# Performance work log

Measured on AMD Instinct MI355X. Metric: run time of the kernel, lower is better.

The kernel has to match this reference:

```python
import jax, jax.numpy as jnp
import numpy as np

HIDDEN = 384
HEADS = 8
DIM_HEAD = HIDDEN // HEADS  # 48
INNER = DIM_HEAD * HEADS
SCALE = DIM_HEAD ** -0.5


def setup_inputs() -> dict:
    key = jax.random.key(0)
    k1, k2, k3, k4 = jax.random.split(key, 4)
    B, C, D, H, W = 2, HIDDEN, 16, 16, 8
    x = jax.random.normal(k1, (B, C, D, H, W), dtype=jnp.float32)
    # nn.Linear weights (stored as [out, in] in torch; use [in, out] here)
    w_qkv = jax.random.normal(k2, (C, 3 * INNER), dtype=jnp.float32) * (C ** -0.5)
    w_out = jax.random.normal(k3, (INNER, C), dtype=jnp.float32) * (INNER ** -0.5)
    b_out = jax.random.normal(k4, (C,), dtype=jnp.float32) * 0.02
    return {"x": x, "w_qkv": w_qkv, "w_out": w_out, "b_out": b_out}


def reference(x, w_qkv, w_out, b_out):
    B, C, D, H, W = x.shape
    N = D * H * W
    tokens = x.reshape(B, C, N).transpose(0, 2, 1)          # [B, N, C]
    qkv = tokens @ w_qkv                                     # [B, N, 3*inner]
    qkv = qkv.reshape(B, N, 3, HEADS, DIM_HEAD).transpose(2, 0, 3, 1, 4)
    q, k, v = qkv[0], qkv[1], qkv[2]                         # [B, h, N, dh]
    q = jnp.clip(q, -5.0, 5.0)
    k = jnp.clip(k, -5.0, 5.0)
    logits = jnp.einsum('bhnd,bhmd->bhnm', q, k) * SCALE     # [B, h, N, N]
    logits = logits - jnp.max(logits, axis=-1, keepdims=True)
    attn = jax.nn.softmax(logits, axis=-1)
    out = jnp.einsum('bhnm,bhmd->bhnd', attn, v)             # [B, h, N, dh]
    out = out.transpose(0, 2, 1, 3).reshape(B, N, INNER)     # [B, N, inner]
    out = out @ w_out + b_out                                # [B, N, C]
    out = out.transpose(0, 2, 1).reshape(B, C, D, H, W)
    return x + out
```

## Files before the change

kernel.cpp:

```cpp
#include <hip/hip_runtime.h>

#define B_SZ 2
#define C_IN 384
#define N_TOK 2048
#define HEADS 8
#define DH 48
#define J3 1152
#define QSCALE_LOG2 0.20823509110768f
#define KSPLIT 4
#define KEYS_PER_SPLIT 512
#define DEFER_THR 11.0f

typedef __attribute__((ext_vector_type(8))) _Float16 f16x8;
typedef __attribute__((ext_vector_type(4))) _Float16 f16x4;
typedef __attribute__((ext_vector_type(4))) float f32x4;

__device__ __forceinline__ unsigned short f2h(float f) {
  _Float16 h = (_Float16)f;
  return __builtin_bit_cast(unsigned short, h);
}
__device__ __forceinline__ uint pk2(float a, float b) {
  return __builtin_bit_cast(uint, __builtin_amdgcn_cvt_pkrtz(a, b));
}
__device__ __forceinline__ float exp2g(float x) {
  return __builtin_amdgcn_exp2f(x);
}

__global__ __launch_bounds__(256) void tr_kernel(
    const float* __restrict__ x, const float* __restrict__ wq,
    const float* __restrict__ wo, unsigned short* __restrict__ xh,
    unsigned short* __restrict__ wqh, unsigned short* __restrict__ woh) {
  const int z = blockIdx.z;
  const float* src;
  unsigned short* dst;
  int C;
  if (z < 2) {
    src = x + (size_t)z * C_IN * N_TOK;
    dst = xh + (size_t)z * N_TOK * C_IN;
    C = N_TOK;
  } else if (z == 2) {
    src = wq; dst = wqh; C = J3;
  } else {
    src = wo; dst = woh; C = C_IN;
  }
  const int c0 = blockIdx.x * 64;
  const int r0 = blockIdx.y * 64;
  if (c0 >= C) return;
  __shared__ unsigned short T[64][74];
  const int tid = threadIdx.x;
  const int cc = tid & 63;
#pragma unroll
  for (int i = 0; i < 16; ++i) {
    const int rr = 4 * i + (tid >> 6);
    T[cc][rr] = f2h(src[(size_t)(r0 + rr) * C + c0 + cc]);
  }
  __syncthreads();
  const int cc2 = tid >> 2;
  const int seg = (tid & 3) * 16;
  uint v[8];
#pragma unroll
  for (int k = 0; k < 8; ++k)
    v[k] = (uint)T[cc2][seg + 2 * k] | ((uint)T[cc2][seg + 2 * k + 1] << 16);
  unsigned short* dp = dst + (size_t)(c0 + cc2) * C_IN + r0 + seg;
  *(uint4*)dp = make_uint4(v[0], v[1], v[2], v[3]);
  *(uint4*)(dp + 8) = make_uint4(v[4], v[5], v[6], v[7]);
}

__global__ __launch_bounds__(256) void qkv_mfma(
    const unsigned short* __restrict__ xh, const unsigned short* __restrict__ wqh,
    unsigned short* __restrict__ Qo, unsigned short* __restrict__ Ko,
    unsigned short* __restrict__ Vo) {
  __shared__ __align__(16) unsigned short Ts[128][72];
  __shared__ __align__(16) unsigned short Ws[64][72];
  const int tid = threadIdx.x;
  const int w = tid >> 6, lane = tid & 63;
  const int lc = lane & 15, lg = lane >> 4;
  const int m0 = blockIdx.x * 128;
  const int j0 = blockIdx.y * 64;
  const int b = m0 >> 11;

  f32x4 acc[2][4];
#pragma unroll
  for (int i = 0; i < 2; ++i)
#pragma unroll
    for (int j = 0; j < 4; ++j) acc[i][j] = (f32x4){0.f, 0.f, 0.f, 0.f};

  const int trow = tid & 127, tseg = tid >> 7;
  const int wrow = tid & 63,  wseg = tid >> 6;

  for (int kk = 0; kk < C_IN; kk += 64) {
    {
      const uint4* s = (const uint4*)(xh + (size_t)(m0 + trow) * C_IN + kk + tseg * 32);
      uint4* d = (uint4*)&Ts[trow][tseg * 32];
      d[0] = s[0]; d[1] = s[1]; d[2] = s[2]; d[3] = s[3];
      const uint4* s2 = (const uint4*)(wqh + (size_t)(j0 + wrow) * C_IN + kk + wseg * 16);
      uint4* d2 = (uint4*)&Ws[wrow][wseg * 16];
      d2[0] = s2[0]; d2[1] = s2[1];
    }
    __syncthreads();
    f16x8 a[2][2], bf[4][2];
#pragma unroll
    for (int mt = 0; mt < 2; ++mt)
#pragma unroll
      for (int kh = 0; kh < 2; ++kh)
        a[mt][kh] = *(const f16x8*)&Ts[32 * w + 16 * mt + lc][32 * kh + 8 * lg];
#pragma unroll
    for (int jt = 0; jt < 4; ++jt)
#pragma unroll
      for (int kh = 0; kh < 2; ++kh)
        bf[jt][kh] = *(const f16x8*)&Ws[16 * jt + lc][32 * kh + 8 * lg];
#pragma unroll
    for (int mt = 0; mt < 2; ++mt)
#pragma unroll
      for (int jt = 0; jt < 4; ++jt)
#pragma unroll
        for (int kh = 0; kh < 2; ++kh)
          acc[mt][jt] = __builtin_amdgcn_mfma_f32_16x16x32_f16(a[mt][kh], bf[jt][kh], acc[mt][jt], 0, 0, 0);
    __syncthreads();
  }

  if (j0 >= 768) {
    unsigned short* Tv = &Ts[0][0];
#pragma unroll
    for (int jt = 0; jt < 4; ++jt)
#pragma unroll
      for (int mt = 0; mt < 2; ++mt)
#pragma unroll
        for (int r = 0; r < 4; ++r)
          Tv[(16 * jt + lc) * 136 + (32 * w + 16 * mt + 4 * lg + r)] =
              f2h(acc[mt][jt][r]);
    __syncthreads();
    const int n0 = m0 & 2047;
#pragma unroll
    for (int i = 0; i < 4; ++i) {
      const int s = tid + i * 256;
      const int row = s >> 4;
      const int segoff = (s & 15) * 8;
      const int rr2 = j0 - 768 + row;
      const int head = rr2 / DH;
      const int d = rr2 - head * DH;
      const int bh = b * HEADS + head;
      *(uint4*)(Vo + ((size_t)bh * DH + d) * N_TOK + n0 + segoff) =
          *(const uint4*)&Tv[row * 136 + segoff];
    }
  } else {
#pragma unroll
    for (int jt = 0; jt < 4; ++jt) {
      const int jlo = j0 + 16 * jt;
      const int which = jlo / 384;
      const int rr = jlo - which * 384;
      const int head = rr / DH;
      const int dbase = rr - head * DH;
      const int d = dbase + lc;
      const int bh = b * HEADS + head;
#pragma unroll
      for (int mt = 0; mt < 2; ++mt)
#pragma unroll
        for (int r = 0; r < 4; ++r) {
          const int n = (m0 + 32 * w + 16 * mt + 4 * lg + r) & 2047;
          float val = fminf(fmaxf(acc[mt][jt][r], -5.f), 5.f);
          if (which == 0) {
            Qo[((size_t)bh * N_TOK + n) * DH + d] = f2h(val * QSCALE_LOG2);
          } else {
            Ko[((size_t)bh * N_TOK + n) * DH + d] = f2h(val);
          }
        }
    }
  }
}

__global__ __launch_bounds__(512) void attn_kernel(
    const unsigned short* __restrict__ Q, const unsigned short* __restrict__ K,
    const unsigned short* __restrict__ Vt, unsigned short* __restrict__ Opart,
    float2* __restrict__ ml) {
  const int qt = blockIdx.x, bh = blockIdx.y, ks = blockIdx.z;
  const int b = bh >> 3, h = bh & 7;
  const int n0 = qt * 128;
  const int tid = threadIdx.x;
  const int w = tid >> 6, lane = tid & 63;
  const int lc = lane & 15, lg = lane >> 4;

  __shared__ __align__(16) unsigned short Ks[2][64][56];
  __shared__ __align__(16) unsigned short Vs[2][48][68];

  const unsigned short* Qrow = Q + ((size_t)bh * N_TOK + n0 + 16 * w + lc) * DH;
  const f16x8 qf0 = *(const f16x8*)(Qrow + 8 * lg);
  f16x8 qf1 = {0, 0, 0, 0, 0, 0, 0, 0};
  {
    const f16x4 t = *(const f16x4*)(Qrow + 32 + 4 * lg);
    qf1[0] = t[0]; qf1[1] = t[1]; qf1[2] = t[2]; qf1[3] = t[3];
  }

  const unsigned short* Kg = K + (size_t)bh * N_TOK * DH + (size_t)ks * KEYS_PER_SPLIT * DH;
  const uint* Vg32 = (const uint*)(Vt + (size_t)bh * DH * N_TOK) + ks * (KEYS_PER_SPLIT / 2);

  uint kr[3], vr[3];
  auto issue = [&](int t0) {
    const uint* Ksrc = (const uint*)(Kg + (size_t)t0 * DH);
#pragma unroll
    for (int i = 0; i < 3; ++i) {
      const int dw = tid + i * 512;
      kr[i] = Ksrc[dw];
      vr[i] = Vg32[(size_t)(dw >> 5) * 1024 + (t0 >> 1) + (dw & 31)];
    }
  };
  auto commit = [&](int buf) {
#pragma unroll
    for (int i = 0; i < 3; ++i) {
      const int dw = tid + i * 512;
      const int key = dw / 24, c = dw - key * 24;
      *(uint*)&Ks[buf][key][2 * c] = kr[i];
      *(uint*)&Vs[buf][dw >> 5][2 * (dw & 31)] = vr[i];
    }
  };

  float m_run = -1e30f, l_run = 0.f;
  f32x4 oacc[3] = {{0,0,0,0},{0,0,0,0},{0,0,0,0}};

  issue(0);
  commit(0);

  for (int t = 0; t < KEYS_PER_SPLIT / 64; ++t) {
    const int cur = t & 1;
    if (t < KEYS_PER_SPLIT / 64 - 1) issue((t + 1) * 64);
    __syncthreads();

    f32x4 sac[4];
    __builtin_amdgcn_s_setprio(1);
#pragma unroll
    for (int it = 0; it < 4; ++it) {
      const int krow = 16 * it + lc;
      const f16x8 kf0 = *(const f16x8*)&Ks[cur][krow][8 * lg];
      f16x8 kf1 = {0, 0, 0, 0, 0, 0, 0, 0};
      const f16x4 tt = *(const f16x4*)&Ks[cur][krow][32 + 4 * lg];
      kf1[0] = tt[0]; kf1[1] = tt[1]; kf1[2] = tt[2]; kf1[3] = tt[3];
      const f32x4 z = {0.f, 0.f, 0.f, 0.f};
      f32x4 s = __builtin_amdgcn_mfma_f32_16x16x32_f16(kf0, qf0, z, 0, 0, 0);
      sac[it]  = __builtin_amdgcn_mfma_f32_16x16x32_f16(kf1, qf1, s, 0, 0, 0);
    }
    __builtin_amdgcn_s_setprio(0);

    float mt = -1e30f;
#pragma unroll
    for (int it = 0; it < 4; ++it)
#pragma unroll
      for (int r = 0; r < 4; ++r) mt = fmaxf(mt, sac[it][r]);
    mt = fmaxf(mt, __shfl_xor(mt, 16, 64));
    mt = fmaxf(mt, __shfl_xor(mt, 32, 64));

    if (!__all(mt - m_run <= DEFER_THR)) {
      const float mn = fmaxf(m_run, mt);
      const float rs = exp2g(m_run - mn);
      m_run = mn;
      l_run *= rs;
#pragma unroll
      for (int itd = 0; itd < 3; ++itd)
#pragma unroll
        for (int r = 0; r < 4; ++r) oacc[itd][r] *= rs;
    }

    float p[4][4];
    float ps = 0.f;
#pragma unroll
    for (int it = 0; it < 4; ++it)
#pragma unroll
      for (int r = 0; r < 4; ++r) {
        p[it][r] = exp2g(sac[it][r] - m_run);
        ps += p[it][r];
      }
    ps += __shfl_xor(ps, 16, 64);
    ps += __shfl_xor(ps, 32, 64);
    l_run += ps;

    f16x8 pt[2];
#pragma unroll
    for (int ks2 = 0; ks2 < 2; ++ks2) {
      union { f16x8 v; uint u[4]; } pu;
      pu.u[0] = pk2(p[2 * ks2][0], p[2 * ks2][1]);
      pu.u[1] = pk2(p[2 * ks2][2], p[2 * ks2][3]);
      pu.u[2] = pk2(p[2 * ks2 + 1][0], p[2 * ks2 + 1][1]);
      pu.u[3] = pk2(p[2 * ks2 + 1][2], p[2 * ks2 + 1][3]);
      pt[ks2] = pu.v;
    }

    __builtin_amdgcn_s_setprio(1);
#pragma unroll
    for (int itd = 0; itd < 3; ++itd) {
      const int drow = 16 * itd + lc;
#pragma unroll
      for (int ks2 = 0; ks2 < 2; ++ks2) {
        const f16x4 v0 = *(const f16x4*)&Vs[cur][drow][4 * lg + 32 * ks2];
        const f16x4 v1 = *(const f16x4*)&Vs[cur][drow][4 * lg + 32 * ks2 + 16];
        f16x8 vf;
        vf[0] = v0[0]; vf[1] = v0[1]; vf[2] = v0[2]; vf[3] = v0[3];
        vf[4] = v1[0]; vf[5] = v1[1]; vf[6] = v1[2]; vf[7] = v1[3];
        oacc[itd] = __builtin_amdgcn_mfma_f32_16x16x32_f16(vf, pt[ks2], oacc[itd], 0, 0, 0);
      }
    }
    __builtin_amdgcn_s_setprio(0);

    if (t < KEYS_PER_SPLIT / 64 - 1) commit(cur ^ 1);
  }

  if (lg == 0)
    ml[(size_t)(ks * 16 + bh) * N_TOK + n0 + 16 * w + lc] = make_float2(m_run, l_run);
  const float inv = 1.f / l_run;
  unsigned short* Ap = Opart +
      ((size_t)(ks * B_SZ + b) * N_TOK + n0 + 16 * w + lc) * 384 + h * DH;
#pragma unroll
  for (int itd = 0; itd < 3; ++itd) {
    uint2 pkv;
    pkv.x = pk2(oacc[itd][0] * inv, oacc[itd][1] * inv);
    pkv.y = pk2(oacc[itd][2] * inv, oacc[itd][3] * inv);
    *(uint2*)(Ap + 16 * itd + 4 * lg) = pkv;
  }
}

__global__ __launch_bounds__(256) void combine_kernel(
    const unsigned short* __restrict__ Opart, const float2* __restrict__ ml,
    unsigned short* __restrict__ AOh) {
  const int vid = blockIdx.x * 256 + threadIdx.x;
  const int c8 = vid % 48;
  const int n  = (vid / 48) & 2047;
  const int b  = vid / (48 * 2048);
  const int c0 = c8 * 8;
  const int h  = c0 / 48;
  const int bh = b * 8 + h;
  const size_t PS = (size_t)B_SZ * N_TOK * 384;
  float2 e0 = ml[(size_t)(0 * 16 + bh) * N_TOK + n];
  float2 e1 = ml[(size_t)(1 * 16 + bh) * N_TOK + n];
  float2 e2 = ml[(size_t)(2 * 16 + bh) * N_TOK + n];
  float2 e3 = ml[(size_t)(3 * 16 + bh) * N_TOK + n];
  const float M = fmaxf(fmaxf(e0.x, e1.x), fmaxf(e2.x, e3.x));
  const float g0 = exp2g(e0.x - M) * e0.y, g1 = exp2g(e1.x - M) * e1.y;
  const float g2 = exp2g(e2.x - M) * e2.y, g3 = exp2g(e3.x - M) * e3.y;
  const float inv = 1.f / (g0 + g1 + g2 + g3);
  const float s0 = g0 * inv, s1 = g1 * inv, s2 = g2 * inv, s3 = g3 * inv;
  const size_t o = ((size_t)b * N_TOK + n) * 384 + c0;
  union U8 { uint4 q; _Float16 e[8]; } u0, u1, u2, u3, r;
  u0.q = *(const uint4*)(Opart + 0 * PS + o);
  u1.q = *(const uint4*)(Opart + 1 * PS + o);
  u2.q = *(const uint4*)(Opart + 2 * PS + o);
  u3.q = *(const uint4*)(Opart + 3 * PS + o);
#pragma unroll
  for (int k = 0; k < 8; k += 2) {
    const float a = (float)u0.e[k] * s0 + (float)u1.e[k] * s1 +
                    (float)u2.e[k] * s2 + (float)u3.e[k] * s3;
    const float bb = (float)u0.e[k + 1] * s0 + (float)u1.e[k + 1] * s1 +
                     (float)u2.e[k + 1] * s2 + (float)u3.e[k + 1] * s3;
    *(uint*)&r.e[k] = pk2(a, bb);
  }
  *(uint4*)(AOh + o) = r.q;
}

__global__ __launch_bounds__(256) void proj_mfma(
    const unsigned short* __restrict__ AOh, const unsigned short* __restrict__ woh,
    const float* __restrict__ b_out, const float* __restrict__ x,
    float* __restrict__ out) {
  __shared__ __align__(16) unsigned short As[64][72];
  __shared__ __align__(16) unsigned short Bs[128][72];
  const int tid = threadIdx.x;
  const int w = tid >> 6, lane = tid & 63;
  const int lc = lane & 15, lg = lane >> 4;
  const int c0 = blockIdx.x * 64;
  const int m0 = blockIdx.y * 128;
  const int b = m0 >> 11;

  f32x4 acc[4][2];
#pragma unroll
  for (int i = 0; i < 4; ++i)
#pragma unroll
    for (int j = 0; j < 2; ++j) acc[i][j] = (f32x4){0.f, 0.f, 0.f, 0.f};

  const int arow = tid & 63,  aseg = tid >> 6;
  const int brow = tid & 127, bseg = tid >> 7;

  for (int kk = 0; kk < C_IN; kk += 64) {
    {
      const uint4* s = (const uint4*)(woh + (size_t)(c0 + arow) * C_IN + kk + aseg * 16);
      uint4* d = (uint4*)&As[arow][aseg * 16];
      d[0] = s[0]; d[1] = s[1];
      const uint4* s2 = (const uint4*)(AOh + (size_t)(m0 + brow) * C_IN + kk + bseg * 32);
      uint4* d2 = (uint4*)&Bs[brow][bseg * 32];
      d2[0] = s2[0]; d2[1] = s2[1]; d2[2] = s2[2]; d2[3] = s2[3];
    }
    __syncthreads();
    f16x8 a[4][2], bf[2][2];
#pragma unroll
    for (int ct = 0; ct < 4; ++ct)
#pragma unroll
      for (int kh = 0; kh < 2; ++kh)
        a[ct][kh] = *(const f16x8*)&As[16 * ct + lc][32 * kh + 8 * lg];
#pragma unroll
    for (int mt = 0; mt < 2; ++mt)
#pragma unroll
      for (int kh = 0; kh < 2; ++kh)
        bf[mt][kh] = *(const f16x8*)&Bs[32 * w + 16 * mt + lc][32 * kh + 8 * lg];
#pragma unroll
    for (int ct = 0; ct < 4; ++ct)
#pragma unroll
      for (int mt = 0; mt < 2; ++mt)
#pragma unroll
        for (int kh = 0; kh < 2; ++kh)
          acc[ct][mt] = __builtin_amdgcn_mfma_f32_16x16x32_f16(a[ct][kh], bf[mt][kh], acc[ct][mt], 0, 0, 0);
    __syncthreads();
  }

#pragma unroll
  for (int ct = 0; ct < 4; ++ct)
#pragma unroll
    for (int r = 0; r < 4; ++r) {
      const int c = c0 + 16 * ct + 4 * lg + r;
      const float bias = b_out[c];
#pragma unroll
      for (int mt = 0; mt < 2; ++mt) {
        const int n = (m0 + 32 * w + 16 * mt + lc) & 2047;
        const size_t off = ((size_t)b * C_IN + c) * N_TOK + n;
        out[off] = x[off] + bias + acc[ct][mt][r];
      }
    }
}

extern "C" void kernel_launch(void* const* d_in, const int* in_sizes, int n_in,
                              void* d_out, int out_size, void* d_ws, size_t ws_size,
                              hipStream_t stream) {
  const float* x     = (const float*)d_in[0];
  const float* w_qkv = (const float*)d_in[1];
  const float* w_out = (const float*)d_in[2];
  const float* b_out = (const float*)d_in[3];
  float* out = (float*)d_out;

  char* ws = (char*)d_ws;
  unsigned short* xh    = (unsigned short*)(ws);
  unsigned short* wqh   = (unsigned short*)(ws + 3145728);
  unsigned short* woh   = (unsigned short*)(ws + 4030464);
  unsigned short* Qb    = (unsigned short*)(ws + 4325376);
  unsigned short* Kb    = (unsigned short*)(ws + 7471104);
  unsigned short* Vb    = (unsigned short*)(ws + 10616832);
  unsigned short* Opart = (unsigned short*)(ws + 13762560);
  float2*         mlb   = (float2*)(ws + 26345472);
  unsigned short* AOh   = (unsigned short*)(ws + 27394048);

  tr_kernel<<<dim3(32, 6, 4), 256, 0, stream>>>(x, w_qkv, w_out, xh, wqh, woh);
  qkv_mfma<<<dim3(32, 18), 256, 0, stream>>>(xh, wqh, Qb, Kb, Vb);
  attn_kernel<<<dim3(16, 16, KSPLIT), 512, 0, stream>>>(Qb, Kb, Vb, Opart, mlb);
  combine_kernel<<<dim3(768), 256, 0, stream>>>(Opart, mlb, AOh);
  proj_mfma<<<dim3(6, 32), 256, 0, stream>>>(AOh, woh, b_out, x, out);
}
```

Baseline: 75.22 us.

## Fuse fp32-to-fp16 transpose into QKV and projection GEMM tile loads

Removes the separate transpose/convert kernel. The QKV and projection GEMMs now read fp32 x and weights directly, convert them to fp16 and transpose them through an extra shared-memory staging buffer inside each K-loop iteration. This drops one kernel launch and the write-then-read round trip of the fp16 copies. In exchange, x and w_qkv are re-read and re-converted by every block that needs them (x by each of the 18 column blocks), each iteration adds a barrier, and the column-wise LDS transposes may hit bank conflicts.

```diff
diff --git a/kernel.cpp b/kernel.cpp
--- a/kernel.cpp
+++ b/kernel.cpp
@@ -26,58 +26,21 @@
   return __builtin_amdgcn_exp2f(x);
 }
 
-__global__ __launch_bounds__(256) void tr_kernel(
+__global__ __launch_bounds__(256) void qkv_mfma(
     const float* __restrict__ x, const float* __restrict__ wq,
-    const float* __restrict__ wo, unsigned short* __restrict__ xh,
-    unsigned short* __restrict__ wqh, unsigned short* __restrict__ woh) {
-  const int z = blockIdx.z;
-  const float* src;
-  unsigned short* dst;
-  int C;
-  if (z < 2) {
-    src = x + (size_t)z * C_IN * N_TOK;
-    dst = xh + (size_t)z * N_TOK * C_IN;
-    C = N_TOK;
-  } else if (z == 2) {
-    src = wq; dst = wqh; C = J3;
-  } else {
-    src = wo; dst = woh; C = C_IN;
-  }
-  const int c0 = blockIdx.x * 64;
-  const int r0 = blockIdx.y * 64;
-  if (c0 >= C) return;
-  __shared__ unsigned short T[64][74];
-  const int tid = threadIdx.x;
-  const int cc = tid & 63;
-#pragma unroll
-  for (int i = 0; i < 16; ++i) {
-    const int rr = 4 * i + (tid >> 6);
-    T[cc][rr] = f2h(src[(size_t)(r0 + rr) * C + c0 + cc]);
-  }
-  __syncthreads();
-  const int cc2 = tid >> 2;
-  const int seg = (tid & 3) * 16;
-  uint v[8];
-#pragma unroll
-  for (int k = 0; k < 8; ++k)
-    v[k] = (uint)T[cc2][seg + 2 * k] | ((uint)T[cc2][seg + 2 * k + 1] << 16);
-  unsigned short* dp = dst + (size_t)(c0 + cc2) * C_IN + r0 + seg;
-  *(uint4*)dp = make_uint4(v[0], v[1], v[2], v[3]);
-  *(uint4*)(dp + 8) = make_uint4(v[4], v[5], v[6], v[7]);
-}
-
-__global__ __launch_bounds__(256) void qkv_mfma(
-    const unsigned short* __restrict__ xh, const unsigned short* __restrict__ wqh,
     unsigned short* __restrict__ Qo, unsigned short* __restrict__ Ko,
     unsigned short* __restrict__ Vo) {
   __shared__ __align__(16) unsigned short Ts[128][72];
   __shared__ __align__(16) unsigned short Ws[64][72];
+  __shared__ __align__(16) unsigned short Xt[64][132];
+  __shared__ __align__(16) unsigned short Wt[64][68];
   const int tid = threadIdx.x;
   const int w = tid >> 6, lane = tid & 63;
   const int lc = lane & 15, lg = lane >> 4;
   const int m0 = blockIdx.x * 128;
   const int j0 = blockIdx.y * 64;
   const int b = m0 >> 11;
+  const int n0 = m0 & 2047;
 
   f32x4 acc[2][4];
 #pragma unroll
@@ -85,19 +48,49 @@
 #pragma unroll
     for (int j = 0; j < 4; ++j) acc[i][j] = (f32x4){0.f, 0.f, 0.f, 0.f};
 
-  const int trow = tid & 127, tseg = tid >> 7;
-  const int wrow = tid & 63,  wseg = tid >> 6;
+  const float* xbase = x + (size_t)b * C_IN * N_TOK + n0;
 
   for (int kk = 0; kk < C_IN; kk += 64) {
+#pragma unroll
+    for (int i = 0; i < 8; ++i) {
+      const int f = tid + 256 * i;
+      const int c = f >> 5, m4 = (f & 31) * 4;
+      const float4 v = *(const float4*)(xbase + (size_t)(kk + c) * N_TOK + m4);
+      ushort4 h;
+      h.x = f2h(v.x); h.y = f2h(v.y); h.z = f2h(v.z); h.w = f2h(v.w);
+      *(ushort4*)&Xt[c][m4] = h;
+    }
+#pragma unroll
+    for (int i = 0; i < 4; ++i) {
+      const int f = tid + 256 * i;
+      const int c = f >> 4, j4 = (f & 15) * 4;
+      const float4 v = *(const float4*)(wq + (size_t)(kk + c) * J3 + j0 + j4);
+      ushort4 h;
+      h.x = f2h(v.x); h.y = f2h(v.y); h.z = f2h(v.z); h.w = f2h(v.w);
+      *(ushort4*)&Wt[c][j4] = h;
+    }
+    __syncthreads();
+
     {
-      const uint4* s = (const uint4*)(xh + (size_t)(m0 + trow) * C_IN + kk + tseg * 32);
-      uint4* d = (uint4*)&Ts[trow][tseg * 32];
-      d[0] = s[0]; d[1] = s[1]; d[2] = s[2]; d[3] = s[3];
-      const uint4* s2 = (const uint4*)(wqh + (size_t)(j0 + wrow) * C_IN + kk + wseg * 16);
-      uint4* d2 = (uint4*)&Ws[wrow][wseg * 16];
-      d2[0] = s2[0]; d2[1] = s2[1];
-    }
-    __syncthreads();
+      const int m = tid >> 1, ks = (tid & 1) * 32;
+      unsigned short tmp[32];
+#pragma unroll
+      for (int j2 = 0; j2 < 32; ++j2) tmp[j2] = Xt[ks + j2][m];
+#pragma unroll
+      for (int j2 = 0; j2 < 8; ++j2)
+        *(ushort4*)&Ts[m][ks + 4 * j2] =
+            make_ushort4(tmp[4 * j2], tmp[4 * j2 + 1], tmp[4 * j2 + 2], tmp[4 * j2 + 3]);
+      const int jj = tid >> 2, ks2 = (tid & 3) * 16;
+      unsigned short tw[16];
+#pragma unroll
+      for (int i2 = 0; i2 < 16; ++i2) tw[i2] = Wt[ks2 + i2][jj];
+#pragma unroll
+      for (int i2 = 0; i2 < 4; ++i2)
+        *(ushort4*)&Ws[jj][ks2 + 4 * i2] =
+            make_ushort4(tw[4 * i2], tw[4 * i2 + 1], tw[4 * i2 + 2], tw[4 * i2 + 3]);
+    }
+    __syncthreads();
+
     f16x8 a[2][2], bf[4][2];
 #pragma unroll
     for (int mt = 0; mt < 2; ++mt)
@@ -130,7 +123,6 @@
           Tv[(16 * jt + lc) * 136 + (32 * w + 16 * mt + 4 * lg + r)] =
               f2h(acc[mt][jt][r]);
     __syncthreads();
-    const int n0 = m0 & 2047;
 #pragma unroll
     for (int i = 0; i < 4; ++i) {
       const int s = tid + i * 256;
@@ -354,11 +346,12 @@
 }
 
 __global__ __launch_bounds__(256) void proj_mfma(
-    const unsigned short* __restrict__ AOh, const unsigned short* __restrict__ woh,
+    const unsigned short* __restrict__ AOh, const float* __restrict__ wo,
     const float* __restrict__ b_out, const float* __restrict__ x,
     float* __restrict__ out) {
   __shared__ __align__(16) unsigned short As[64][72];
   __shared__ __align__(16) unsigned short Bs[128][72];
+  __shared__ __align__(16) unsigned short Wt2[64][68];
   const int tid = threadIdx.x;
   const int w = tid >> 6, lane = tid & 63;
   const int lc = lane & 15, lg = lane >> 4;
@@ -372,19 +365,37 @@
 #pragma unroll
     for (int j = 0; j < 2; ++j) acc[i][j] = (f32x4){0.f, 0.f, 0.f, 0.f};
 
-  const int arow = tid & 63,  aseg = tid >> 6;
   const int brow = tid & 127, bseg = tid >> 7;
 
   for (int kk = 0; kk < C_IN; kk += 64) {
+#pragma unroll
+    for (int i = 0; i < 4; ++i) {
+      const int f = tid + 256 * i;
+      const int c = f >> 4, c4 = (f & 15) * 4;
+      const float4 v = *(const float4*)(wo + (size_t)(kk + c) * C_IN + c0 + c4);
+      ushort4 h;
+      h.x = f2h(v.x); h.y = f2h(v.y); h.z = f2h(v.z); h.w = f2h(v.w);
+      *(ushort4*)&Wt2[c][c4] = h;
+    }
     {
-      const uint4* s = (const uint4*)(woh + (size_t)(c0 + arow) * C_IN + kk + aseg * 16);
-      uint4* d = (uint4*)&As[arow][aseg * 16];
-      d[0] = s[0]; d[1] = s[1];
       const uint4* s2 = (const uint4*)(AOh + (size_t)(m0 + brow) * C_IN + kk + bseg * 32);
       uint4* d2 = (uint4*)&Bs[brow][bseg * 32];
       d2[0] = s2[0]; d2[1] = s2[1]; d2[2] = s2[2]; d2[3] = s2[3];
     }
     __syncthreads();
+
+    {
+      const int cc = tid >> 2, ks2 = (tid & 3) * 16;
+      unsigned short tw[16];
+#pragma unroll
+      for (int i2 = 0; i2 < 16; ++i2) tw[i2] = Wt2[ks2 + i2][cc];
+#pragma unroll
+      for (int i2 = 0; i2 < 4; ++i2)
+        *(ushort4*)&As[cc][ks2 + 4 * i2] =
+            make_ushort4(tw[4 * i2], tw[4 * i2 + 1], tw[4 * i2 + 2], tw[4 * i2 + 3]);
+    }
+    __syncthreads();
+
     f16x8 a[4][2], bf[2][2];
 #pragma unroll
     for (int ct = 0; ct < 4; ++ct)
@@ -431,19 +442,15 @@
   float* out = (float*)d_out;
 
   char* ws = (char*)d_ws;
-  unsigned short* xh    = (unsigned short*)(ws);
-  unsigned short* wqh   = (unsigned short*)(ws + 3145728);
-  unsigned short* woh   = (unsigned short*)(ws + 4030464);
-  unsigned short* Qb    = (unsigned short*)(ws + 4325376);
-  unsigned short* Kb    = (unsigned short*)(ws + 7471104);
-  unsigned short* Vb    = (unsigned short*)(ws + 10616832);
-  unsigned short* Opart = (unsigned short*)(ws + 13762560);
-  float2*         mlb   = (float2*)(ws + 26345472);
-  unsigned short* AOh   = (unsigned short*)(ws + 27394048);
-
-  tr_kernel<<<dim3(32, 6, 4), 256, 0, stream>>>(x, w_qkv, w_out, xh, wqh, woh);
-  qkv_mfma<<<dim3(32, 18), 256, 0, stream>>>(xh, wqh, Qb, Kb, Vb);
+  unsigned short* Qb    = (unsigned short*)(ws);
+  unsigned short* Kb    = (unsigned short*)(ws + 3145728);
+  unsigned short* Vb    = (unsigned short*)(ws + 6291456);
+  unsigned short* Opart = (unsigned short*)(ws + 9437184);
+  float2*         mlb   = (float2*)(ws + 22020096);
+  unsigned short* AOh   = (unsigned short*)(ws + 23068672);
+
+  qkv_mfma<<<dim3(32, 18), 256, 0, stream>>>(x, w_qkv, Qb, Kb, Vb);
   attn_kernel<<<dim3(16, 16, KSPLIT), 512, 0, stream>>>(Qb, Kb, Vb, Opart, mlb);
   combine_kernel<<<dim3(768), 256, 0, stream>>>(Opart, mlb, AOh);
-  proj_mfma<<<dim3(6, 32), 256, 0, stream>>>(AOh, woh, b_out, x, out);
-}
+  proj_mfma<<<dim3(6, 32), 256, 0, stream>>>(AOh, w_out, b_out, x, out);
+}
```

Measured after the change: 71.59 us. -4.8%, faster.
